# Kernel optimization log

Measured on AMD Instinct MI355X. Metric: run time of the kernel, lower is better.

## Reference

```python
import jax, jax.numpy as jnp
import numpy as np

B = 2048      # number of scenes (samples)
A = 64        # max agents per scene
D = 128       # latent_size (embed dim)
H = 4         # heads (hardcoded in module)
HD = D // H   # head dim = 32
NEG = -1e9


def setup_inputs() -> dict:
    key = jax.random.key(0)
    k1, k2, k3, k4 = jax.random.split(key, 4)
    # flat ragged agent features; only the first sum(agents) rows are 'real'
    att_in = jax.random.normal(k1, (B * A, D), dtype=jnp.float32)
    agents_per_sample = jax.random.randint(k2, (B,), 1, A + 1)  # each scene has >=1 agent
    s = 1.0 / np.sqrt(D)
    w_in = jax.random.uniform(k3, (3 * D, D), minval=-s, maxval=s, dtype=jnp.float32)
    b_in = jnp.zeros((3 * D,), dtype=jnp.float32)
    w_out = jax.random.uniform(k4, (D, D), minval=-s, maxval=s, dtype=jnp.float32)
    b_out = jnp.zeros((D,), dtype=jnp.float32)
    return {"att_in": att_in, "w_in": w_in, "b_in": b_in,
            "w_out": w_out, "b_out": b_out, "agents_per_sample": agents_per_sample}


def reference(att_in, w_in, b_in, w_out, b_out, agents_per_sample):
    # scatter flat ragged rows into padded [B, A, D] (same as padded_att_in[mask] = att_in)
    offsets = jnp.cumsum(agents_per_sample) - agents_per_sample          # exclusive prefix sum
    idx = offsets[:, None] + jnp.arange(A)[None, :]                      # [B, A] flat row index
    mask = jnp.arange(A)[None, :] < agents_per_sample[:, None]          # [B, A] valid-agent mask
    padded = jnp.take(att_in, idx, axis=0) * mask[..., None].astype(att_in.dtype)
    # fused in-projection (nn.MultiheadAttention in_proj)
    qkv = padded @ w_in.T + b_in                                        # [B, A, 3D]
    q, k, v = jnp.split(qkv, 3, axis=-1)
    q = q.reshape(B, A, H, HD)
    k = k.reshape(B, A, H, HD)
    v = v.reshape(B, A, H, HD)
    scores = jnp.einsum('bqhd,bkhd->bhqk', q, k) / np.sqrt(HD).astype(q.dtype)
    # key_padding_mask: padded keys excluded from softmax
    scores = jnp.where(mask[:, None, None, :], scores, NEG)
    attn = jax.nn.softmax(scores, axis=-1)
    ctx = jnp.einsum('bhqk,bkhd->bqhd', attn, v).reshape(B, A, D)
    out = (ctx @ w_out.T + b_out) * mask[..., None].astype(ctx.dtype)   # zero out padded rows (torch slices them off)
    return out
```

## Files before the change

### kernel.cpp

```cpp
#include <hip/hip_runtime.h>
#include <hip/hip_bf16.h>

typedef __bf16 bf16;
typedef __bf16 bf16x4 __attribute__((ext_vector_type(4)));
typedef __bf16 bf16x8 __attribute__((ext_vector_type(8)));
typedef float  f32x4  __attribute__((ext_vector_type(4)));

#define NEG_INF (-1e9f)
#define N_SCENES 2048

__global__ __launch_bounds__(256) void prep_kernel(
    const float* __restrict__ w_in, const float* __restrict__ w_out,
    const int* __restrict__ agents,
    bf16* __restrict__ w_in_b, bf16* __restrict__ w_out_b, int* __restrict__ offs)
{
    __shared__ int tot[256];
    const int t = threadIdx.x;
    if (blockIdx.x == 0) {
        int loc[8]; int s = 0;
        #pragma unroll
        for (int j = 0; j < 8; ++j) { loc[j] = agents[t * 8 + j]; s += loc[j]; }
        tot[t] = s;
        __syncthreads();
        for (int o = 1; o < 256; o <<= 1) {
            int v = (t >= o) ? tot[t - o] : 0;
            __syncthreads();
            tot[t] += v;
            __syncthreads();
        }
        int run = tot[t] - s;
        #pragma unroll
        for (int j = 0; j < 8; ++j) { offs[t * 8 + j] = run; run += loc[j]; }
    } else {
        int i = (blockIdx.x - 1) * 1024 + t * 4;
        float4 v; bf16* dst;
        if (i < 49152) { v = *(const float4*)(w_in + i);            dst = w_in_b + i; }
        else           { v = *(const float4*)(w_out + (i - 49152)); dst = w_out_b + (i - 49152); }
        bf16x4 o = { (bf16)v.x, (bf16)v.y, (bf16)v.z, (bf16)v.w };
        *(bf16x4*)dst = o;
    }
}

__global__ __launch_bounds__(256, 3) void attn_kernel(
    const float* __restrict__ att_in,
    const float* __restrict__ b_in, const float* __restrict__ b_out,
    const bf16* __restrict__ w_in_b, const bf16* __restrict__ w_out_b,
    const int* __restrict__ agents, const int* __restrict__ offs,
    float* __restrict__ out)
{
    __shared__ bf16 s_lds[4 * 6144];

    const int b    = blockIdx.x;
    const int tid  = threadIdx.x;
    const int lane = tid & 63;
    const int w    = tid >> 6;
    const int h    = w;
    const int r    = lane & 15;
    const int qd   = lane >> 4;
    const int q1   = qd & 1;
    const int qh   = qd >> 1;
    const int nb   = agents[b];
    const int off  = offs[b];
    const int mtc  = (nb + 15) >> 4;

    bf16* Qld = s_lds + w * 6144;
    bf16* Kld = Qld + 2048;
    bf16* vT  = Qld + 4096;

    {
        const float4 z4 = make_float4(0.f, 0.f, 0.f, 0.f);
        const int nz = (64 - nb) * 32;
        for (int i = tid; i < nz; i += 256) {
            int row = nb + (i >> 5);
            *(float4*)(out + ((size_t)b * 64 + row) * 128 + (i & 31) * 4) = z4;
        }
    }

    {
        bf16x4 z4 = {(bf16)0.f,(bf16)0.f,(bf16)0.f,(bf16)0.f};
        int zrow = lane >> 1, zh = lane & 1;
        #pragma unroll
        for (int u = 2; u < 8; ++u)
            if (u >= 2 * mtc) {
                int uu = u ^ (zrow & 7);
                *(bf16x4*)(vT + zrow * 64 + uu * 8 + zh * 4) = z4;
            }
    }

    bf16x8 xa[4][4];
    #pragma unroll
    for (int mt = 0; mt < 4; ++mt) {
        const int xrow = mt * 16 + r;
        const bool vr = xrow < nb;
        const float* px = att_in + (((size_t)(off + xrow)) << 7) + qd * 8;
        #pragma unroll
        for (int ks = 0; ks < 4; ++ks) {
            float4 lo = make_float4(0.f,0.f,0.f,0.f), hi = lo;
            if (vr) {
                lo = *(const float4*)(px + ks * 32);
                hi = *(const float4*)(px + ks * 32 + 4);
            }
            xa[mt][ks] = (bf16x8){(bf16)lo.x,(bf16)lo.y,(bf16)lo.z,(bf16)lo.w,
                                  (bf16)hi.x,(bf16)hi.y,(bf16)hi.z,(bf16)hi.w};
        }
    }

    #pragma unroll
    for (int t = 0; t < 6; ++t) {
        const int kind = t >> 1, jt = t & 1;
        const int j0 = kind * 128 + h * 32 + jt * 16;
        const bf16* pw = w_in_b + (size_t)(j0 + r) * 128 + qd * 8;
        bf16x8 wb[4];
        #pragma unroll
        for (int ks = 0; ks < 4; ++ks)
            wb[ks] = *(const bf16x8*)(pw + ks * 32);
        if (kind < 2) {
            const float4 b4 = *(const float4*)(b_in + j0 + qd * 4);
            bf16* dst = (kind == 0) ? Qld : Kld;
            #pragma unroll
            for (int mt = 0; mt < 4; ++mt)
                if (mt < mtc) {
                    f32x4 acc = {0.f,0.f,0.f,0.f};
                    #pragma unroll
                    for (int ks = 0; ks < 4; ++ks)
                        acc = __builtin_amdgcn_mfma_f32_16x16x32_bf16(wb[ks], xa[mt][ks], acc, 0, 0, 0);
                    bf16x4 pk = {(bf16)(acc[0]+b4.x), (bf16)(acc[1]+b4.y),
                                 (bf16)(acc[2]+b4.z), (bf16)(acc[3]+b4.w)};
                    int rowa = mt * 16 + r;
                    int uu = (jt * 2 + qh) ^ (rowa & 3);
                    *(bf16x4*)(dst + rowa * 32 + uu * 8 + q1 * 4) = pk;
                }
        } else {
            const float bv = b_in[j0 + r];
            #pragma unroll
            for (int mt = 0; mt < 4; ++mt)
                if (mt < mtc) {
                    f32x4 acc = {0.f,0.f,0.f,0.f};
                    #pragma unroll
                    for (int ks = 0; ks < 4; ++ks)
                        acc = __builtin_amdgcn_mfma_f32_16x16x32_bf16(xa[mt][ks], wb[ks], acc, 0, 0, 0);
                    bf16x4 pk = {(bf16)(acc[0]+bv), (bf16)(acc[1]+bv),
                                 (bf16)(acc[2]+bv), (bf16)(acc[3]+bv)};
                    int rowd = jt * 16 + r;
                    int uu = (mt * 2 + qh) ^ (rowd & 7);
                    *(bf16x4*)(vT + rowd * 64 + uu * 8 + q1 * 4) = pk;
                }
        }
    }

    bf16x8 kf[4];
    #pragma unroll
    for (int nt = 0; nt < 4; ++nt)
        if (nt < mtc) {
            int row = nt * 16 + r;
            kf[nt] = *(const bf16x8*)(Kld + row * 32 + (qd ^ (row & 3)) * 8);
        }
    bf16x8 vf[2][2];
    #pragma unroll
    for (int dt = 0; dt < 2; ++dt)
        #pragma unroll
        for (int hk = 0; hk < 2; ++hk) {
            int row = dt * 16 + r;
            vf[dt][hk] = *(const bf16x8*)(vT + row * 64 + ((hk * 4 + qd) ^ (row & 7)) * 8);
        }
    bf16x8 wof[2][4]; float4 bo4[2];
    #pragma unroll
    for (int t2 = 0; t2 < 2; ++t2) {
        const int jg = (w * 2 + t2) * 16;
        const bf16* pw = w_out_b + (size_t)(jg + r) * 128 + qd * 8;
        #pragma unroll
        for (int s = 0; s < 4; ++s)
            wof[t2][s] = *(const bf16x8*)(pw + s * 32);
        bo4[t2] = *(const float4*)(b_out + jg + qd * 4);
    }

    const float scale = 0.17677669529663687f;

    #pragma unroll
    for (int mt = 0; mt < 4; ++mt)
        if (mt < mtc) {
            int qrow = mt * 16 + r;
            bf16x8 qf = *(const bf16x8*)(Qld + qrow * 32 + (qd ^ (qrow & 3)) * 8);
            f32x4 S[4];
            #pragma unroll
            for (int nt = 0; nt < 4; ++nt)
                if (nt < mtc) {
                    f32x4 z = {0.f,0.f,0.f,0.f};
                    S[nt] = __builtin_amdgcn_mfma_f32_16x16x32_bf16(kf[nt], qf, z, 0, 0, 0);
                }
            float mx = NEG_INF;
            #pragma unroll
            for (int nt = 0; nt < 4; ++nt) {
                if (nt < mtc) {
                    #pragma unroll
                    for (int i = 0; i < 4; ++i) {
                        bool kv = (nt * 16 + qd * 4 + i) < nb;
                        float val = kv ? S[nt][i] * scale : NEG_INF;
                        S[nt][i] = val;
                        mx = fmaxf(mx, val);
                    }
                } else {
                    S[nt] = (f32x4){NEG_INF, NEG_INF, NEG_INF, NEG_INF};
                }
            }
            mx = fmaxf(mx, __shfl_xor(mx, 16));
            mx = fmaxf(mx, __shfl_xor(mx, 32));
            float l = 0.f;
            #pragma unroll
            for (int nt = 0; nt < 4; ++nt)
                #pragma unroll
                for (int i = 0; i < 4; ++i) {
                    float e = __expf(S[nt][i] - mx);
                    S[nt][i] = e; l += e;
                }
            l += __shfl_xor(l, 16);
            l += __shfl_xor(l, 32);
            const float rl = 1.0f / l;
            #pragma unroll
            for (int nt = 0; nt < 4; ++nt)
                #pragma unroll
                for (int i = 0; i < 4; ++i)
                    S[nt][i] *= rl;

            f32x4 o0 = {0.f,0.f,0.f,0.f}, o1 = {0.f,0.f,0.f,0.f};
            #pragma unroll
            for (int hk = 0; hk < 2; ++hk)
                if (hk * 2 < mtc) {
                    float pv[8];
                    #pragma unroll
                    for (int jj = 0; jj < 8; ++jj) {
                        int sl = r + q1 * 32 + (jj >> 2) * 16;
                        float f0 = __shfl(S[2*hk  ][jj & 3], sl);
                        float f1 = __shfl(S[2*hk+1][jj & 3], sl);
                        pv[jj] = (qd < 2) ? f0 : f1;
                    }
                    bf16x8 pf = {(bf16)pv[0],(bf16)pv[1],(bf16)pv[2],(bf16)pv[3],
                                 (bf16)pv[4],(bf16)pv[5],(bf16)pv[6],(bf16)pv[7]};
                    o0 = __builtin_amdgcn_mfma_f32_16x16x32_bf16(vf[0][hk], pf, o0, 0, 0, 0);
                    o1 = __builtin_amdgcn_mfma_f32_16x16x32_bf16(vf[1][hk], pf, o1, 0, 0, 0);
                }

            float cv[8];
            #pragma unroll
            for (int jj = 0; jj < 8; ++jj) {
                int sl = r + q1 * 32 + (jj >> 2) * 16;
                float f0 = __shfl(o0[jj & 3], sl);
                float f1 = __shfl(o1[jj & 3], sl);
                cv[jj] = (qd < 2) ? f0 : f1;
            }
            bf16x8 cf = {(bf16)cv[0],(bf16)cv[1],(bf16)cv[2],(bf16)cv[3],
                         (bf16)cv[4],(bf16)cv[5],(bf16)cv[6],(bf16)cv[7]};
            *(bf16x8*)(Qld + mt * 512 + lane * 8) = cf;
        }
    __syncthreads();

    #pragma unroll
    for (int mt = 0; mt < 4; ++mt)
        if (mt < mtc) {
            bf16x8 cb[4];
            #pragma unroll
            for (int s = 0; s < 4; ++s)
                cb[s] = *(const bf16x8*)(s_lds + s * 6144 + mt * 512 + lane * 8);
            const int rowa = mt * 16 + r;
            #pragma unroll
            for (int t2 = 0; t2 < 2; ++t2) {
                f32x4 acc = {0.f,0.f,0.f,0.f};
                #pragma unroll
                for (int s = 0; s < 4; ++s)
                    acc = __builtin_amdgcn_mfma_f32_16x16x32_bf16(wof[t2][s], cb[s], acc, 0, 0, 0);
                if (rowa < nb) {
                    float4 o4 = make_float4(acc[0] + bo4[t2].x, acc[1] + bo4[t2].y,
                                            acc[2] + bo4[t2].z, acc[3] + bo4[t2].w);
                    *(float4*)(out + ((size_t)b * 64 + rowa) * 128
                               + (w * 2 + t2) * 16 + qd * 4) = o4;
                }
            }
        }
}

extern "C" void kernel_launch(void* const* d_in, const int* in_sizes, int n_in,
                              void* d_out, int out_size, void* d_ws, size_t ws_size,
                              hipStream_t stream)
{
    const float* att_in = (const float*)d_in[0];
    const float* w_in   = (const float*)d_in[1];
    const float* b_in   = (const float*)d_in[2];
    const float* w_out  = (const float*)d_in[3];
    const float* b_out  = (const float*)d_in[4];
    const int*   agents = (const int*)d_in[5];

    bf16* w_in_b  = (bf16*)d_ws;
    bf16* w_out_b = w_in_b + 49152;
    int*  offs    = (int*)((char*)d_ws + 98304 + 32768);

    prep_kernel<<<65, 256, 0, stream>>>(w_in, w_out, agents, w_in_b, w_out_b, offs);
    attn_kernel<<<N_SCENES, 256, 0, stream>>>(att_in, b_in, b_out, w_in_b, w_out_b,
                                              agents, offs, (float*)d_out);
}
```

Measured before the change: 176.8 us.

## Sort scenes by agent count and keep Q/K fragments in registers

The prep kernel now counting-sorts scene indices by descending agent count, so the attention grid processes the largest scenes first and load balance across the GPU improves. Q and K projections are redistributed into MFMA operand fragments with lane shuffles instead of a round trip through LDS. That shrinks per-block LDS from 48KB to 16KB, and occupancy is raised to 4 blocks. The input projection is processed in pairs of row tiles to cap register use. The risks are register pressure at the higher occupancy and the added shuffle work.

```diff
diff --git a/kernel.cpp b/kernel.cpp
--- a/kernel.cpp
+++ b/kernel.cpp
@@ -12,11 +12,15 @@
 __global__ __launch_bounds__(256) void prep_kernel(
     const float* __restrict__ w_in, const float* __restrict__ w_out,
     const int* __restrict__ agents,
-    bf16* __restrict__ w_in_b, bf16* __restrict__ w_out_b, int* __restrict__ offs)
+    bf16* __restrict__ w_in_b, bf16* __restrict__ w_out_b,
+    int* __restrict__ offs, int* __restrict__ perm)
 {
     __shared__ int tot[256];
+    __shared__ int cnt[65];
+    __shared__ int start[65];
     const int t = threadIdx.x;
     if (blockIdx.x == 0) {
+        if (t < 65) cnt[t] = 0;
         int loc[8]; int s = 0;
         #pragma unroll
         for (int j = 0; j < 8; ++j) { loc[j] = agents[t * 8 + j]; s += loc[j]; }
@@ -31,6 +35,19 @@
         int run = tot[t] - s;
         #pragma unroll
         for (int j = 0; j < 8; ++j) { offs[t * 8 + j] = run; run += loc[j]; }
+        #pragma unroll
+        for (int j = 0; j < 8; ++j) atomicAdd(&cnt[loc[j]], 1);
+        __syncthreads();
+        if (t == 0) {
+            int pos = 0;
+            for (int v = 64; v >= 1; --v) { start[v] = pos; pos += cnt[v]; }
+        }
+        __syncthreads();
+        #pragma unroll
+        for (int j = 0; j < 8; ++j) {
+            int p = atomicAdd(&start[loc[j]], 1);
+            perm[p] = t * 8 + j;
+        }
     } else {
         int i = (blockIdx.x - 1) * 1024 + t * 4;
         float4 v; bf16* dst;
@@ -41,38 +58,37 @@
     }
 }
 
-__global__ __launch_bounds__(256, 3) void attn_kernel(
+__global__ __launch_bounds__(256, 4) void attn_kernel(
     const float* __restrict__ att_in,
     const float* __restrict__ b_in, const float* __restrict__ b_out,
     const bf16* __restrict__ w_in_b, const bf16* __restrict__ w_out_b,
     const int* __restrict__ agents, const int* __restrict__ offs,
-    float* __restrict__ out)
+    const int* __restrict__ perm, float* __restrict__ out)
 {
-    __shared__ bf16 s_lds[4 * 6144];
-
-    const int b    = blockIdx.x;
-    const int tid  = threadIdx.x;
-    const int lane = tid & 63;
-    const int w    = tid >> 6;
-    const int h    = w;
-    const int r    = lane & 15;
-    const int qd   = lane >> 4;
-    const int q1   = qd & 1;
-    const int qh   = qd >> 1;
-    const int nb   = agents[b];
-    const int off  = offs[b];
-    const int mtc  = (nb + 15) >> 4;
-
-    bf16* Qld = s_lds + w * 6144;
-    bf16* Kld = Qld + 2048;
-    bf16* vT  = Qld + 4096;
+    __shared__ bf16 s_lds[4 * 2048];
+
+    const int b     = blockIdx.x;
+    const int tid   = threadIdx.x;
+    const int lane  = tid & 63;
+    const int w     = tid >> 6;
+    const int h     = w;
+    const int r     = lane & 15;
+    const int qd    = lane >> 4;
+    const int q1    = qd & 1;
+    const int qh    = qd >> 1;
+    const int scene = perm[b];
+    const int nb    = agents[scene];
+    const int off   = offs[scene];
+    const int mtc   = (nb + 15) >> 4;
+
+    bf16* mylds = s_lds + w * 2048;
 
     {
         const float4 z4 = make_float4(0.f, 0.f, 0.f, 0.f);
         const int nz = (64 - nb) * 32;
         for (int i = tid; i < nz; i += 256) {
             int row = nb + (i >> 5);
-            *(float4*)(out + ((size_t)b * 64 + row) * 128 + (i & 31) * 4) = z4;
+            *(float4*)(out + ((size_t)scene * 64 + row) * 128 + (i & 31) * 4) = z4;
         }
     }
 
@@ -83,110 +99,118 @@
         for (int u = 2; u < 8; ++u)
             if (u >= 2 * mtc) {
                 int uu = u ^ (zrow & 7);
-                *(bf16x4*)(vT + zrow * 64 + uu * 8 + zh * 4) = z4;
+                *(bf16x4*)(mylds + zrow * 64 + uu * 8 + zh * 4) = z4;
             }
     }
 
-    bf16x8 xa[4][4];
-    #pragma unroll
-    for (int mt = 0; mt < 4; ++mt) {
-        const int xrow = mt * 16 + r;
-        const bool vr = xrow < nb;
-        const float* px = att_in + (((size_t)(off + xrow)) << 7) + qd * 8;
-        #pragma unroll
-        for (int ks = 0; ks < 4; ++ks) {
-            float4 lo = make_float4(0.f,0.f,0.f,0.f), hi = lo;
-            if (vr) {
-                lo = *(const float4*)(px + ks * 32);
-                hi = *(const float4*)(px + ks * 32 + 4);
-            }
-            xa[mt][ks] = (bf16x8){(bf16)lo.x,(bf16)lo.y,(bf16)lo.z,(bf16)lo.w,
-                                  (bf16)hi.x,(bf16)hi.y,(bf16)hi.z,(bf16)hi.w};
-        }
-    }
-
-    #pragma unroll
-    for (int t = 0; t < 6; ++t) {
-        const int kind = t >> 1, jt = t & 1;
-        const int j0 = kind * 128 + h * 32 + jt * 16;
-        const bf16* pw = w_in_b + (size_t)(j0 + r) * 128 + qd * 8;
-        bf16x8 wb[4];
-        #pragma unroll
-        for (int ks = 0; ks < 4; ++ks)
-            wb[ks] = *(const bf16x8*)(pw + ks * 32);
-        if (kind < 2) {
-            const float4 b4 = *(const float4*)(b_in + j0 + qd * 4);
-            bf16* dst = (kind == 0) ? Qld : Kld;
-            #pragma unroll
-            for (int mt = 0; mt < 4; ++mt)
-                if (mt < mtc) {
-                    f32x4 acc = {0.f,0.f,0.f,0.f};
+    bf16x8 qB[4], kA[4];
+    #pragma unroll
+    for (int pr = 0; pr < 2; ++pr)
+        if (pr * 2 < mtc) {
+            bf16x8 xa[2][4];
+            #pragma unroll
+            for (int ms = 0; ms < 2; ++ms) {
+                const int mt = pr * 2 + ms;
+                const int xrow = mt * 16 + r;
+                const bool vr = xrow < nb;
+                const float* px = att_in + (((size_t)(off + xrow)) << 7) + qd * 8;
+                #pragma unroll
+                for (int ks = 0; ks < 4; ++ks) {
+                    float4 lo = make_float4(0.f,0.f,0.f,0.f), hi = lo;
+                    if (vr) {
+                        lo = *(const float4*)(px + ks * 32);
+                        hi = *(const float4*)(px + ks * 32 + 4);
+                    }
+                    xa[ms][ks] = (bf16x8){(bf16)lo.x,(bf16)lo.y,(bf16)lo.z,(bf16)lo.w,
+                                          (bf16)hi.x,(bf16)hi.y,(bf16)hi.z,(bf16)hi.w};
+                }
+            }
+            #pragma unroll
+            for (int kind = 0; kind < 2; ++kind) {
+                f32x4 C[2][2];
+                #pragma unroll
+                for (int jt = 0; jt < 2; ++jt) {
+                    const int j0 = kind * 128 + h * 32 + jt * 16;
+                    const bf16* pw = w_in_b + (size_t)(j0 + r) * 128 + qd * 8;
+                    bf16x8 wb[4];
                     #pragma unroll
                     for (int ks = 0; ks < 4; ++ks)
-                        acc = __builtin_amdgcn_mfma_f32_16x16x32_bf16(wb[ks], xa[mt][ks], acc, 0, 0, 0);
-                    bf16x4 pk = {(bf16)(acc[0]+b4.x), (bf16)(acc[1]+b4.y),
-                                 (bf16)(acc[2]+b4.z), (bf16)(acc[3]+b4.w)};
-                    int rowa = mt * 16 + r;
-                    int uu = (jt * 2 + qh) ^ (rowa & 3);
-                    *(bf16x4*)(dst + rowa * 32 + uu * 8 + q1 * 4) = pk;
-                }
-        } else {
-            const float bv = b_in[j0 + r];
-            #pragma unroll
-            for (int mt = 0; mt < 4; ++mt)
-                if (mt < mtc) {
-                    f32x4 acc = {0.f,0.f,0.f,0.f};
-                    #pragma unroll
-                    for (int ks = 0; ks < 4; ++ks)
-                        acc = __builtin_amdgcn_mfma_f32_16x16x32_bf16(xa[mt][ks], wb[ks], acc, 0, 0, 0);
-                    bf16x4 pk = {(bf16)(acc[0]+bv), (bf16)(acc[1]+bv),
-                                 (bf16)(acc[2]+bv), (bf16)(acc[3]+bv)};
-                    int rowd = jt * 16 + r;
-                    int uu = (mt * 2 + qh) ^ (rowd & 7);
-                    *(bf16x4*)(vT + rowd * 64 + uu * 8 + q1 * 4) = pk;
-                }
-        }
-    }
-
-    bf16x8 kf[4];
-    #pragma unroll
-    for (int nt = 0; nt < 4; ++nt)
-        if (nt < mtc) {
-            int row = nt * 16 + r;
-            kf[nt] = *(const bf16x8*)(Kld + row * 32 + (qd ^ (row & 3)) * 8);
-        }
+                        wb[ks] = *(const bf16x8*)(pw + ks * 32);
+                    const float4 b4 = *(const float4*)(b_in + j0 + qd * 4);
+                    #pragma unroll
+                    for (int ms = 0; ms < 2; ++ms) {
+                        f32x4 acc = {0.f,0.f,0.f,0.f};
+                        #pragma unroll
+                        for (int ks = 0; ks < 4; ++ks)
+                            acc = __builtin_amdgcn_mfma_f32_16x16x32_bf16(wb[ks], xa[ms][ks], acc, 0, 0, 0);
+                        acc[0] += b4.x; acc[1] += b4.y; acc[2] += b4.z; acc[3] += b4.w;
+                        C[ms][jt] = acc;
+                    }
+                }
+                #pragma unroll
+                for (int ms = 0; ms < 2; ++ms) {
+                    const int mt = pr * 2 + ms;
+                    float tv[8];
+                    #pragma unroll
+                    for (int jj = 0; jj < 8; ++jj) {
+                        int sl = r + q1 * 32 + (jj >> 2) * 16;
+                        float f0 = __shfl(C[ms][0][jj & 3], sl);
+                        float f1 = __shfl(C[ms][1][jj & 3], sl);
+                        tv[jj] = (qd < 2) ? f0 : f1;
+                    }
+                    bf16x8 fr = {(bf16)tv[0],(bf16)tv[1],(bf16)tv[2],(bf16)tv[3],
+                                 (bf16)tv[4],(bf16)tv[5],(bf16)tv[6],(bf16)tv[7]};
+                    if (kind == 0) qB[mt] = fr; else kA[mt] = fr;
+                }
+            }
+            #pragma unroll
+            for (int jt = 0; jt < 2; ++jt) {
+                const int j0 = 256 + h * 32 + jt * 16;
+                const bf16* pw = w_in_b + (size_t)(j0 + r) * 128 + qd * 8;
+                bf16x8 wb[4];
+                #pragma unroll
+                for (int ks = 0; ks < 4; ++ks)
+                    wb[ks] = *(const bf16x8*)(pw + ks * 32);
+                const float bv = b_in[j0 + r];
+                #pragma unroll
+                for (int ms = 0; ms < 2; ++ms) {
+                    const int mt = pr * 2 + ms;
+                    if (mt < mtc) {
+                        f32x4 acc = {0.f,0.f,0.f,0.f};
+                        #pragma unroll
+                        for (int ks = 0; ks < 4; ++ks)
+                            acc = __builtin_amdgcn_mfma_f32_16x16x32_bf16(xa[ms][ks], wb[ks], acc, 0, 0, 0);
+                        const int rowd = jt * 16 + r;
+                        const int uu = (mt * 2 + qh) ^ (rowd & 7);
+                        bf16x4 pk = {(bf16)(acc[0]+bv), (bf16)(acc[1]+bv),
+                                     (bf16)(acc[2]+bv), (bf16)(acc[3]+bv)};
+                        *(bf16x4*)(mylds + rowd * 64 + uu * 8 + q1 * 4) = pk;
+                    }
+                }
+            }
+        }
+
     bf16x8 vf[2][2];
     #pragma unroll
     for (int dt = 0; dt < 2; ++dt)
         #pragma unroll
         for (int hk = 0; hk < 2; ++hk) {
             int row = dt * 16 + r;
-            vf[dt][hk] = *(const bf16x8*)(vT + row * 64 + ((hk * 4 + qd) ^ (row & 7)) * 8);
-        }
-    bf16x8 wof[2][4]; float4 bo4[2];
-    #pragma unroll
-    for (int t2 = 0; t2 < 2; ++t2) {
-        const int jg = (w * 2 + t2) * 16;
-        const bf16* pw = w_out_b + (size_t)(jg + r) * 128 + qd * 8;
-        #pragma unroll
-        for (int s = 0; s < 4; ++s)
-            wof[t2][s] = *(const bf16x8*)(pw + s * 32);
-        bo4[t2] = *(const float4*)(b_out + jg + qd * 4);
-    }
+            vf[dt][hk] = *(const bf16x8*)(mylds + row * 64 + ((hk * 4 + qd) ^ (row & 7)) * 8);
+        }
 
     const float scale = 0.17677669529663687f;
+    const int hkc = (mtc + 1) >> 1;
 
     #pragma unroll
     for (int mt = 0; mt < 4; ++mt)
         if (mt < mtc) {
-            int qrow = mt * 16 + r;
-            bf16x8 qf = *(const bf16x8*)(Qld + qrow * 32 + (qd ^ (qrow & 3)) * 8);
             f32x4 S[4];
             #pragma unroll
             for (int nt = 0; nt < 4; ++nt)
                 if (nt < mtc) {
                     f32x4 z = {0.f,0.f,0.f,0.f};
-                    S[nt] = __builtin_amdgcn_mfma_f32_16x16x32_bf16(kf[nt], qf, z, 0, 0, 0);
+                    S[nt] = __builtin_amdgcn_mfma_f32_16x16x32_bf16(kA[nt], qB[mt], z, 0, 0, 0);
                 }
             float mx = NEG_INF;
             #pragma unroll
@@ -225,7 +249,7 @@
             f32x4 o0 = {0.f,0.f,0.f,0.f}, o1 = {0.f,0.f,0.f,0.f};
             #pragma unroll
             for (int hk = 0; hk < 2; ++hk)
-                if (hk * 2 < mtc) {
+                if (hk < hkc) {
                     float pv[8];
                     #pragma unroll
                     for (int jj = 0; jj < 8; ++jj) {
@@ -250,8 +274,19 @@
             }
             bf16x8 cf = {(bf16)cv[0],(bf16)cv[1],(bf16)cv[2],(bf16)cv[3],
                          (bf16)cv[4],(bf16)cv[5],(bf16)cv[6],(bf16)cv[7]};
-            *(bf16x8*)(Qld + mt * 512 + lane * 8) = cf;
-        }
+            *(bf16x8*)(mylds + mt * 512 + lane * 8) = cf;
+        }
+
+    bf16x8 wof[2][4]; float4 bo4[2];
+    #pragma unroll
+    for (int t2 = 0; t2 < 2; ++t2) {
+        const int jg = (w * 2 + t2) * 16;
+        const bf16* pw = w_out_b + (size_t)(jg + r) * 128 + qd * 8;
+        #pragma unroll
+        for (int s = 0; s < 4; ++s)
+            wof[t2][s] = *(const bf16x8*)(pw + s * 32);
+        bo4[t2] = *(const float4*)(b_out + jg + qd * 4);
+    }
     __syncthreads();
 
     #pragma unroll
@@ -260,7 +295,7 @@
             bf16x8 cb[4];
             #pragma unroll
             for (int s = 0; s < 4; ++s)
-                cb[s] = *(const bf16x8*)(s_lds + s * 6144 + mt * 512 + lane * 8);
+                cb[s] = *(const bf16x8*)(s_lds + s * 2048 + mt * 512 + lane * 8);
             const int rowa = mt * 16 + r;
             #pragma unroll
             for (int t2 = 0; t2 < 2; ++t2) {
@@ -271,7 +306,7 @@
                 if (rowa < nb) {
                     float4 o4 = make_float4(acc[0] + bo4[t2].x, acc[1] + bo4[t2].y,
                                             acc[2] + bo4[t2].z, acc[3] + bo4[t2].w);
-                    *(float4*)(out + ((size_t)b * 64 + rowa) * 128
+                    *(float4*)(out + ((size_t)scene * 64 + rowa) * 128
                                + (w * 2 + t2) * 16 + qd * 4) = o4;
                 }
             }
@@ -291,9 +326,10 @@
 
     bf16* w_in_b  = (bf16*)d_ws;
     bf16* w_out_b = w_in_b + 49152;
-    int*  offs    = (int*)((char*)d_ws + 98304 + 32768);
-
-    prep_kernel<<<65, 256, 0, stream>>>(w_in, w_out, agents, w_in_b, w_out_b, offs);
+    int*  offs    = (int*)((char*)d_ws + 131072);
+    int*  perm    = (int*)((char*)d_ws + 131072 + 8192);
+
+    prep_kernel<<<65, 256, 0, stream>>>(w_in, w_out, agents, w_in_b, w_out_b, offs, perm);
     attn_kernel<<<N_SCENES, 256, 0, stream>>>(att_in, b_in, b_out, w_in_b, w_out_b,
-                                              agents, offs, (float*)d_out);
+                                              agents, offs, perm, (float*)d_out);
 }
```

Result: slower. 217.2 us (+22.8%).
